# Kernel tuning notes

Hardware: AMD Instinct MI355X
Metric: run time of the kernel (lower is better)

The kernel has to match this reference:

```python
import jax, jax.numpy as jnp
import numpy as np

B, T, C = 2, 2048, 768
NH = 12
HS = C // NH


def setup_inputs() -> dict:
    key = jax.random.key(0)
    k1, k2, k3 = jax.random.split(key, 3)
    x = jax.random.normal(k1, (B, T, C), dtype=jnp.float32)
    # c_attn: Linear(C, 3C). Stored as (C, 3C) so y = x @ w + b (same math as torch x @ W.T + b).
    w_attn = jax.random.normal(k2, (C, 3 * C), dtype=jnp.float32) * (1.0 / np.sqrt(C))
    b_attn = jax.random.normal(k3, (3 * C,), dtype=jnp.float32) * 0.02
    return {"x": x, "w_attn": w_attn, "b_attn": b_attn}


def reference(x, w_attn, b_attn):
    b, t, c = x.shape
    qkv = x @ w_attn + b_attn                      # [B, T, 3C]
    q, k, v = jnp.split(qkv, 3, axis=-1)
    # [B, T, C] -> [B, NH, T, HS]
    q = q.reshape(b, t, NH, HS).transpose(0, 2, 1, 3)
    k = k.reshape(b, t, NH, HS).transpose(0, 2, 1, 3)
    v = v.reshape(b, t, NH, HS).transpose(0, 2, 1, 3)
    scale = 1.0 / np.sqrt(HS).astype(np.float32)
    wei = jnp.einsum("bhqd,bhkd->bhqk", q, k) * scale   # [B, NH, T, T]
    causal = jnp.tril(jnp.ones((t, t), dtype=bool))
    wei = jnp.where(causal[None, None, :, :], wei, -jnp.inf)
    wei = jax.nn.softmax(wei, axis=-1)
    out = jnp.einsum("bhqk,bhkd->bhqd", wei, v)          # [B, NH, T, HS]
    # NOTE: original module returns here, before head-merge / output projection.
    return out
```

## Files before the change

kernel.cpp:

```cpp
#include <hip/hip_runtime.h>

typedef __bf16 bf16_t;
typedef __bf16 bf16x8 __attribute__((ext_vector_type(8)));
typedef __bf16 bf16x4 __attribute__((ext_vector_type(4)));
typedef _Float16 f16x2 __attribute__((ext_vector_type(2)));
typedef _Float16 f16x4 __attribute__((ext_vector_type(4)));
typedef _Float16 f16x8 __attribute__((ext_vector_type(8)));
typedef float f32x4 __attribute__((ext_vector_type(4)));

#define B_   2
#define T_   2048
#define C_   768
#define NH_  12
#define HS_  64
#define N3_  2304
#define M_   4096
#define QSCALE 0.18033688011112042f

__device__ __forceinline__ bf16_t f2bf(float f) {
  unsigned u = __builtin_bit_cast(unsigned, f);
  u += 0x7fffu + ((u >> 16) & 1u);
  unsigned short s = (unsigned short)(u >> 16);
  return __builtin_bit_cast(bf16_t, s);
}

__global__ __launch_bounds__(256) void cvt_xw_kernel(const float* __restrict__ x,
                                                     const float* __restrict__ w,
                                                     bf16_t* __restrict__ xb,
                                                     bf16_t* __restrict__ wt) {
  __shared__ float tile[32][33];
  int bx = blockIdx.x;
  if (bx < 3072) {
    int i = (bx * 256 + threadIdx.x) * 4;
    float4 v = *reinterpret_cast<const float4*>(x + i);
    xb[i + 0] = f2bf(v.x);
    xb[i + 1] = f2bf(v.y);
    xb[i + 2] = f2bf(v.z);
    xb[i + 3] = f2bf(v.w);
  } else {
    int b = bx - 3072;
    int k0 = (b % 24) * 32, n0 = (b / 24) * 32;
    int tx = threadIdx.x & 31, ty = threadIdx.x >> 5;
#pragma unroll
    for (int i = 0; i < 4; i++)
      tile[ty + i * 8][tx] = w[(size_t)(k0 + ty + i * 8) * N3_ + n0 + tx];
    __syncthreads();
#pragma unroll
    for (int i = 0; i < 4; i++)
      wt[(size_t)(n0 + ty + i * 8) * C_ + k0 + tx] = f2bf(tile[tx][ty + i * 8]);
  }
}

__global__ __launch_bounds__(256) void gemm_qkv(const bf16_t* __restrict__ xb,
                                                const bf16_t* __restrict__ wt,
                                                const float* __restrict__ bias,
                                                bf16_t* __restrict__ qout,
                                                bf16_t* __restrict__ kout,
                                                _Float16* __restrict__ va) {
  __shared__ bf16_t As[2][64 * 32];
  __shared__ bf16_t Bs[2][128 * 32];
  const int tid = threadIdx.x;
  const int lane = tid & 63, wave = tid >> 6;
  const int wm = wave >> 1, wn = wave & 1;
  const int quad = lane >> 4, l15 = lane & 15;
  const int row0 = blockIdx.y * 64;
  const int col0 = blockIdx.x * 128;
  const bool isqk = (col0 < 1536);

  f32x4 acc[2][4];
#pragma unroll
  for (int mi = 0; mi < 2; mi++)
#pragma unroll
    for (int ni = 0; ni < 4; ni++) acc[mi][ni] = f32x4{0.f, 0.f, 0.f, 0.f};

  const int r0 = tid >> 2, q0 = tid & 3;
  const int r1 = (256 + tid) >> 2, q1 = (256 + tid) & 3;
  const bf16_t* gA0 = xb + (size_t)(row0 + r0) * C_ + q0 * 8;
  const bf16_t* gB0 = wt + (size_t)(col0 + r0) * C_ + q0 * 8;
  const bf16_t* gB1 = wt + (size_t)(col0 + r1) * C_ + q1 * 8;
  const int ldsOff0 = (wave * 64) * 16;
  const int ldsOff1 = (256 + wave * 64) * 16;

  auto STAGE = [&](int buf, int k0) {
    __builtin_amdgcn_global_load_lds((const __attribute__((address_space(1))) void*)(gA0 + k0),
                                     (__attribute__((address_space(3))) void*)((char*)As[buf] + ldsOff0), 16, 0, 0);
    __builtin_amdgcn_global_load_lds((const __attribute__((address_space(1))) void*)(gB0 + k0),
                                     (__attribute__((address_space(3))) void*)((char*)Bs[buf] + ldsOff0), 16, 0, 0);
    __builtin_amdgcn_global_load_lds((const __attribute__((address_space(1))) void*)(gB1 + k0),
                                     (__attribute__((address_space(3))) void*)((char*)Bs[buf] + ldsOff1), 16, 0, 0);
  };

  STAGE(0, 0);
  __syncthreads();

  constexpr int NT = C_ / 32;
#pragma unroll 2
  for (int t = 0; t < NT; ++t) {
    const int cur = t & 1;
    if (t + 1 < NT) STAGE(cur ^ 1, (t + 1) * 32);

    bf16x8 af[2], bfr[4];
#pragma unroll
    for (int mi = 0; mi < 2; mi++)
      af[mi] = *reinterpret_cast<const bf16x8*>(&As[cur][(wm * 32 + mi * 16 + l15) * 32 + quad * 8]);
#pragma unroll
    for (int ni = 0; ni < 4; ni++)
      bfr[ni] = *reinterpret_cast<const bf16x8*>(&Bs[cur][(wn * 64 + ni * 16 + l15) * 32 + quad * 8]);
    if (isqk) {
#pragma unroll
      for (int mi = 0; mi < 2; mi++)
#pragma unroll
        for (int ni = 0; ni < 4; ni++)
          acc[mi][ni] = __builtin_amdgcn_mfma_f32_16x16x32_bf16(bfr[ni], af[mi], acc[mi][ni], 0, 0, 0);
    } else {
#pragma unroll
      for (int mi = 0; mi < 2; mi++)
#pragma unroll
        for (int ni = 0; ni < 4; ni++)
          acc[mi][ni] = __builtin_amdgcn_mfma_f32_16x16x32_bf16(af[mi], bfr[ni], acc[mi][ni], 0, 0, 0);
    }
    __syncthreads();
  }

  if (isqk) {
#pragma unroll
    for (int mi = 0; mi < 2; mi++) {
      int t = row0 + wm * 32 + mi * 16 + l15;
      int b = t >> 11, tt = t & 2047;
#pragma unroll
      for (int ni = 0; ni < 4; ni++) {
        int cN0 = col0 + wn * 64 + ni * 16 + quad * 4;
        int which = cN0 / 768;
        int rem = cN0 - which * 768;
        int h = rem >> 6, d0 = rem & 63;
        float4 bv = *reinterpret_cast<const float4*>(bias + cN0);
        float sc = which ? 1.0f : QSCALE;
        bf16x4 pack;
        pack[0] = f2bf((acc[mi][ni][0] + bv.x) * sc);
        pack[1] = f2bf((acc[mi][ni][1] + bv.y) * sc);
        pack[2] = f2bf((acc[mi][ni][2] + bv.z) * sc);
        pack[3] = f2bf((acc[mi][ni][3] + bv.w) * sc);
        bf16_t* dst = which ? kout : qout;
        *reinterpret_cast<bf16x4*>(dst + (((size_t)b * NH_ + h) * T_ + tt) * HS_ + d0) = pack;
      }
    }
  } else {
#pragma unroll
    for (int mi = 0; mi < 2; mi++) {
      int trow = row0 + wm * 32 + mi * 16 + quad * 4;
      int b = trow >> 11, tt = trow & 2047;
      int kt = tt >> 6, nj = (tt >> 4) & 3, qd = (tt >> 2) & 3;
#pragma unroll
      for (int ni = 0; ni < 4; ni++) {
        int cN = col0 + wn * 64 + ni * 16 + l15;
        int rem = cN - 1536;
        int h = rem >> 6, d = rem & 63;
        int bh = b * NH_ + h;
        float bv = bias[cN];
        f16x4 pk;
#pragma unroll
        for (int r = 0; r < 4; r++) pk[r] = (_Float16)(acc[mi][ni][r] + bv);
        size_t off = ((((((size_t)bh * 32 + kt) * 4 + nj) * 4 + qd) * 16 + (d & 15)) * 16) + (d >> 4) * 4;
        *reinterpret_cast<f16x4*>(va + off) = pk;
      }
    }
  }
}

__global__ __launch_bounds__(256) void attn_kernel(const bf16_t* __restrict__ qb,
                                                   const bf16_t* __restrict__ kb,
                                                   const _Float16* __restrict__ va,
                                                   float* __restrict__ out) {
  __shared__ bf16_t Ks[2][64][72];
  __shared__ _Float16 Vs[2][4][2][64][8];
  const int tid = threadIdx.x;
  const int lane = tid & 63, wave = tid >> 6;
  const int quad = lane >> 4, l15 = lane & 15;
  const int id = (int)blockIdx.x;
  const int xcd = id & 7, within = id >> 3;
  const int bh = xcd * 3 + within / 16;
  const int pairIdx = within & 15;
  const bf16_t* Qg = qb + (size_t)bh * T_ * HS_;
  const bf16_t* Kg = kb + (size_t)bh * T_ * HS_;
  const _Float16* Vg = va + (size_t)bh * 32 * 4096;

  const int krow = tid >> 2, kcol = (tid & 3) * 16;
  const int vni = tid >> 6, vlane = tid & 63;

  int4 rk0, rk1, rv0, rv1;
  const char* kp;
  const char* vp;
  auto GLOAD = [&]() {
    rk0 = *reinterpret_cast<const int4*>(kp);
    rk1 = *reinterpret_cast<const int4*>(kp + 16);
    rv0 = *reinterpret_cast<const int4*>(vp);
    rv1 = *reinterpret_cast<const int4*>(vp + 16);
    kp += 8192; vp += 8192;
  };
  auto SSTORE = [&](int buf) {
    char* kd = (char*)&Ks[buf][krow][kcol];
    *reinterpret_cast<int4*>(kd) = rk0;
    *reinterpret_cast<int4*>(kd + 16) = rk1;
    *reinterpret_cast<int4*>(&Vs[buf][vni][0][vlane][0]) = rv0;
    *reinterpret_cast<int4*>(&Vs[buf][vni][1][vlane][0]) = rv1;
  };

#pragma unroll
  for (int part = 0; part < 2; part++) {
    const int qtile = part ? pairIdx : 31 - pairIdx;
    const int qrow_base = qtile * 64 + wave * 16;
    const int qmax = qrow_base + 15;
    const int qcol = qrow_base + l15;
    const int nkt = qtile + 1;

    bf16x8 bq0 = *reinterpret_cast<const bf16x8*>(Qg + (size_t)qcol * HS_ + quad * 8);
    bf16x8 bq1 = *reinterpret_cast<const bf16x8*>(Qg + (size_t)qcol * HS_ + 32 + quad * 8);

    float lsum = 0.f;
    f32x4 Oacc[4];
#pragma unroll
    for (int mi = 0; mi < 4; mi++) Oacc[mi] = f32x4{0.f, 0.f, 0.f, 0.f};

    kp = (const char*)Kg + krow * 128 + kcol * 2;
    vp = (const char*)Vg + tid * 32;
    GLOAD();
    __syncthreads();
    SSTORE(0);
    __syncthreads();

    for (int kt = 0; kt < nkt; kt++) {
      const int cur = kt & 1;
      const bool last = (kt + 1 >= nkt);
      if (!last) GLOAD();

      const bool diag = (kt == nkt - 1);
      f16x4 pf[4];
#pragma unroll
      for (int ni = 0; ni < 4; ni++) {
        if (diag && (kt * 64 + ni * 16 > qmax)) continue;
        bf16x8 ka0 = *reinterpret_cast<const bf16x8*>(&Ks[cur][ni * 16 + l15][quad * 8]);
        bf16x8 ka1 = *reinterpret_cast<const bf16x8*>(&Ks[cur][ni * 16 + l15][32 + quad * 8]);
        f32x4 s = {0.f, 0.f, 0.f, 0.f};
        s = __builtin_amdgcn_mfma_f32_16x16x32_bf16(ka0, bq0, s, 0, 0, 0);
        s = __builtin_amdgcn_mfma_f32_16x16x32_bf16(ka1, bq1, s, 0, 0, 0);
        float p0 = __builtin_amdgcn_exp2f(s[0]);
        float p1 = __builtin_amdgcn_exp2f(s[1]);
        float p2 = __builtin_amdgcn_exp2f(s[2]);
        float p3 = __builtin_amdgcn_exp2f(s[3]);
        if (diag) {
          int jb = kt * 64 + ni * 16 + quad * 4;
          if (jb + 0 > qcol) p0 = 0.f;
          if (jb + 1 > qcol) p1 = 0.f;
          if (jb + 2 > qcol) p2 = 0.f;
          if (jb + 3 > qcol) p3 = 0.f;
        }
        lsum += (p0 + p1) + (p2 + p3);
        f16x2 lo2 = __builtin_bit_cast(f16x2, __builtin_amdgcn_cvt_pkrtz(p0, p1));
        f16x2 hi2 = __builtin_bit_cast(f16x2, __builtin_amdgcn_cvt_pkrtz(p2, p3));
        pf[ni] = f16x4{lo2[0], lo2[1], hi2[0], hi2[1]};
      }
#pragma unroll
      for (int ni = 0; ni < 4; ni++) {
        if (diag && (kt * 64 + ni * 16 > qmax)) continue;
#pragma unroll
        for (int p = 0; p < 2; p++) {
          f16x8 vv = *reinterpret_cast<const f16x8*>(&Vs[cur][ni][p][lane][0]);
          f16x4 lo = __builtin_shufflevector(vv, vv, 0, 1, 2, 3);
          f16x4 hi = __builtin_shufflevector(vv, vv, 4, 5, 6, 7);
          Oacc[2 * p]     = __builtin_amdgcn_mfma_f32_16x16x16f16(lo, pf[ni], Oacc[2 * p], 0, 0, 0);
          Oacc[2 * p + 1] = __builtin_amdgcn_mfma_f32_16x16x16f16(hi, pf[ni], Oacc[2 * p + 1], 0, 0, 0);
        }
      }

      if (!last) {
        SSTORE(1 - cur);
        __syncthreads();
      }
    }

    lsum += __shfl_xor(lsum, 16, 64);
    lsum += __shfl_xor(lsum, 32, 64);
    float rinv = 1.0f / lsum;

#pragma unroll
    for (int mi = 0; mi < 4; mi++) {
      float4 o;
      o.x = Oacc[mi][0] * rinv;
      o.y = Oacc[mi][1] * rinv;
      o.z = Oacc[mi][2] * rinv;
      o.w = Oacc[mi][3] * rinv;
      *reinterpret_cast<float4*>(out + ((size_t)bh * T_ + qcol) * HS_ + mi * 16 + quad * 4) = o;
    }
  }
}

extern "C" void kernel_launch(void* const* d_in, const int* in_sizes, int n_in,
                              void* d_out, int out_size, void* d_ws, size_t ws_size,
                              hipStream_t stream) {
  const float* x = (const float*)d_in[0];
  const float* w = (const float*)d_in[1];
  const float* bias = (const float*)d_in[2];
  float* out = (float*)d_out;

  char* ws = (char*)d_ws;
  bf16_t* xb = (bf16_t*)(ws);
  bf16_t* wt = (bf16_t*)(ws + 6291456);
  bf16_t* qb = (bf16_t*)(ws + 6291456 + 3538944);
  bf16_t* kb = qb + 3145728;
  _Float16* va = (_Float16*)(kb + 3145728);

  cvt_xw_kernel<<<dim3(3072 + 1728), dim3(256), 0, stream>>>(x, w, xb, wt);
  gemm_qkv<<<dim3(N3_ / 128, M_ / 64), dim3(256), 0, stream>>>(xb, wt, bias, qb, kb, va);
  attn_kernel<<<dim3(384), dim3(256), 0, stream>>>(qb, kb, va, out);
}
```

Measured before the change: 143.3 us.

## Load K and V tiles directly from global into registers, dropping LDS staging

Removes the shared-memory double buffer and block-wide barriers in the attention loop. Each wave now loads its K fragments straight from global memory into registers, prefetching one tile ahead with ping-pong register arrays, and loads V fragments directly per tile. This removes LDS writes, reads and syncs. In exchange each of the four waves reads the same K/V data separately, relying on L1/L2 for reuse, and register pressure rises.

```diff
diff --git a/kernel.cpp b/kernel.cpp
--- a/kernel.cpp
+++ b/kernel.cpp
@@ -171,8 +171,6 @@
                                                    const bf16_t* __restrict__ kb,
                                                    const _Float16* __restrict__ va,
                                                    float* __restrict__ out) {
-  __shared__ bf16_t Ks[2][64][72];
-  __shared__ _Float16 Vs[2][4][2][64][8];
   const int tid = threadIdx.x;
   const int lane = tid & 63, wave = tid >> 6;
   const int quad = lane >> 4, l15 = lane & 15;
@@ -184,25 +182,18 @@
   const bf16_t* Kg = kb + (size_t)bh * T_ * HS_;
   const _Float16* Vg = va + (size_t)bh * 32 * 4096;
 
-  const int krow = tid >> 2, kcol = (tid & 3) * 16;
-  const int vni = tid >> 6, vlane = tid & 63;
-
-  int4 rk0, rk1, rv0, rv1;
-  const char* kp;
-  const char* vp;
-  auto GLOAD = [&]() {
-    rk0 = *reinterpret_cast<const int4*>(kp);
-    rk1 = *reinterpret_cast<const int4*>(kp + 16);
-    rv0 = *reinterpret_cast<const int4*>(vp);
-    rv1 = *reinterpret_cast<const int4*>(vp + 16);
-    kp += 8192; vp += 8192;
-  };
-  auto SSTORE = [&](int buf) {
-    char* kd = (char*)&Ks[buf][krow][kcol];
-    *reinterpret_cast<int4*>(kd) = rk0;
-    *reinterpret_cast<int4*>(kd + 16) = rk1;
-    *reinterpret_cast<int4*>(&Vs[buf][vni][0][vlane][0]) = rv0;
-    *reinterpret_cast<int4*>(&Vs[buf][vni][1][vlane][0]) = rv1;
+  const int koff = l15 * HS_ + quad * 8;
+  const int voff = lane * 16;
+
+  bf16x8 kA[4][2], kB[4][2];
+
+  auto KLOAD = [&](bf16x8 (&kk)[4][2], int kt) {
+    const bf16_t* Kt = Kg + (size_t)kt * 64 * HS_;
+#pragma unroll
+    for (int ni = 0; ni < 4; ni++) {
+      kk[ni][0] = *reinterpret_cast<const bf16x8*>(Kt + ni * 16 * HS_ + koff);
+      kk[ni][1] = *reinterpret_cast<const bf16x8*>(Kt + ni * 16 * HS_ + koff + 32);
+    }
   };
 
 #pragma unroll
@@ -221,28 +212,22 @@
 #pragma unroll
     for (int mi = 0; mi < 4; mi++) Oacc[mi] = f32x4{0.f, 0.f, 0.f, 0.f};
 
-    kp = (const char*)Kg + krow * 128 + kcol * 2;
-    vp = (const char*)Vg + tid * 32;
-    GLOAD();
-    __syncthreads();
-    SSTORE(0);
-    __syncthreads();
-
-    for (int kt = 0; kt < nkt; kt++) {
-      const int cur = kt & 1;
-      const bool last = (kt + 1 >= nkt);
-      if (!last) GLOAD();
-
+    auto TILE = [&](bf16x8 (&kk)[4][2], int kt) {
       const bool diag = (kt == nkt - 1);
+      const _Float16* Vt = Vg + (size_t)kt * 4096;
+      f16x8 vR[4][2];
+#pragma unroll
+      for (int ni = 0; ni < 4; ni++) {
+        vR[ni][0] = *reinterpret_cast<const f16x8*>(Vt + ni * 1024 + voff);
+        vR[ni][1] = *reinterpret_cast<const f16x8*>(Vt + ni * 1024 + voff + 8);
+      }
       f16x4 pf[4];
 #pragma unroll
       for (int ni = 0; ni < 4; ni++) {
         if (diag && (kt * 64 + ni * 16 > qmax)) continue;
-        bf16x8 ka0 = *reinterpret_cast<const bf16x8*>(&Ks[cur][ni * 16 + l15][quad * 8]);
-        bf16x8 ka1 = *reinterpret_cast<const bf16x8*>(&Ks[cur][ni * 16 + l15][32 + quad * 8]);
         f32x4 s = {0.f, 0.f, 0.f, 0.f};
-        s = __builtin_amdgcn_mfma_f32_16x16x32_bf16(ka0, bq0, s, 0, 0, 0);
-        s = __builtin_amdgcn_mfma_f32_16x16x32_bf16(ka1, bq1, s, 0, 0, 0);
+        s = __builtin_amdgcn_mfma_f32_16x16x32_bf16(kk[ni][0], bq0, s, 0, 0, 0);
+        s = __builtin_amdgcn_mfma_f32_16x16x32_bf16(kk[ni][1], bq1, s, 0, 0, 0);
         float p0 = __builtin_amdgcn_exp2f(s[0]);
         float p1 = __builtin_amdgcn_exp2f(s[1]);
         float p2 = __builtin_amdgcn_exp2f(s[2]);
@@ -264,18 +249,26 @@
         if (diag && (kt * 64 + ni * 16 > qmax)) continue;
 #pragma unroll
         for (int p = 0; p < 2; p++) {
-          f16x8 vv = *reinterpret_cast<const f16x8*>(&Vs[cur][ni][p][lane][0]);
+          f16x8 vv = vR[ni][p];
           f16x4 lo = __builtin_shufflevector(vv, vv, 0, 1, 2, 3);
           f16x4 hi = __builtin_shufflevector(vv, vv, 4, 5, 6, 7);
           Oacc[2 * p]     = __builtin_amdgcn_mfma_f32_16x16x16f16(lo, pf[ni], Oacc[2 * p], 0, 0, 0);
           Oacc[2 * p + 1] = __builtin_amdgcn_mfma_f32_16x16x16f16(hi, pf[ni], Oacc[2 * p + 1], 0, 0, 0);
         }
       }
-
-      if (!last) {
-        SSTORE(1 - cur);
-        __syncthreads();
-      }
+    };
+
+    KLOAD(kA, 0);
+    int kt = 0;
+    while (true) {
+      if (kt + 1 < nkt) KLOAD(kB, kt + 1);
+      TILE(kA, kt);
+      kt++;
+      if (kt >= nkt) break;
+      if (kt + 1 < nkt) KLOAD(kA, kt + 1);
+      TILE(kB, kt);
+      kt++;
+      if (kt >= nkt) break;
     }
 
     lsum += __shfl_xor(lsum, 16, 64);
```

After: 183.3 us. +27.9%, slower.
